# Performance work log

Measured on AMD Instinct MI355X. Metric: run time of the kernel, lower is better.

## Reference

```python
import jax, jax.numpy as jnp
import numpy as np

N, E, R = 50000, 320000, 3
IN, HID, OUT = 768, 256, 64
NEG_SLOPE = 0.2


def _rgat_conv(x, src, dst, edge_type, W, q, k, bias):
    # x: [N, HID]; W: [R, HID, HID]; q,k: [HID, 1]; bias: [HID]
    n = x.shape[0]
    xw = jnp.einsum('nc,rco->rno', x, W)          # [R, N, HID] per-relation transform
    out_i = xw[edge_type, dst]                      # [E, HID] transformed target feats
    out_j = xw[edge_type, src]                      # [E, HID] transformed source feats
    alpha = jax.nn.leaky_relu(out_i @ q + out_j @ k, NEG_SLOPE)  # [E, 1]
    # across-relation segment softmax over destination nodes (PyG softmax semantics)
    m = jax.ops.segment_max(alpha, dst, num_segments=n)          # [N, 1]
    ea = jnp.exp(alpha - m[dst])
    denom = jax.ops.segment_sum(ea, dst, num_segments=n)         # [N, 1]
    a = ea / (denom[dst] + 1e-16)                                # [E, 1]
    out = jax.ops.segment_sum(a * out_j, dst, num_segments=n)    # [N, HID]
    return out + bias


def setup_inputs() -> dict:
    key = jax.random.key(0)
    ks = jax.random.split(key, 16)
    g = lambda k, shape, fan: (jax.random.normal(k, shape, jnp.float32) / np.float32(np.sqrt(fan)))
    return {
        'x': jax.random.normal(ks[0], (N, IN), jnp.float32),
        'edge_index': jax.random.randint(ks[1], (2, E), 0, N),
        'edge_type': jax.random.randint(ks[2], (E,), 0, R),
        'w_in': g(ks[3], (IN, HID), IN), 'b_in': jnp.zeros((HID,), jnp.float32),
        'conv1_w': g(ks[4], (R, HID, HID), HID),
        'conv1_q': g(ks[5], (HID, 1), HID),
        'conv1_k': g(ks[6], (HID, 1), HID),
        'conv1_b': jnp.zeros((HID,), jnp.float32),
        'conv2_w': g(ks[7], (R, HID, HID), HID),
        'conv2_q': g(ks[8], (HID, 1), HID),
        'conv2_k': g(ks[9], (HID, 1), HID),
        'conv2_b': jnp.zeros((HID,), jnp.float32),
        'w_out': g(ks[10], (HID, OUT), HID), 'b_out': jnp.zeros((OUT,), jnp.float32),
        'w_cls': g(ks[11], (OUT, 2), OUT), 'b_cls': jnp.zeros((2,), jnp.float32),
    }


def reference(x, edge_index, edge_type, w_in, b_in,
              conv1_w, conv1_q, conv1_k, conv1_b,
              conv2_w, conv2_q, conv2_k, conv2_b,
              w_out, b_out, w_cls, b_cls):
    src, dst = edge_index[0], edge_index[1]
    h = jax.nn.relu(x @ w_in + b_in)                                  # [N, HID]
    h = _rgat_conv(h, src, dst, edge_type, conv1_w, conv1_q, conv1_k, conv1_b)
    h = _rgat_conv(h, src, dst, edge_type, conv2_w, conv2_q, conv2_k, conv2_b)
    h = jax.nn.relu(h @ w_out + b_out)                                # [N, OUT]
    return h @ w_cls + b_cls                                          # [N, 2]
```

## Files before the change

kernel.cpp:

```cpp
#include <hip/hip_runtime.h>
#include <hip/hip_bf16.h>

#define RG86_NN 50000
#define RG86_NE 320000
#define RG86_NR 3
#define RG86_DIN 768
#define RG86_HID 256
#define RG86_OUT 64

typedef __bf16 rg_bv8 __attribute__((ext_vector_type(8)));
typedef short rg_sv8 __attribute__((ext_vector_type(8)));
typedef float rg_fv4 __attribute__((ext_vector_type(4)));
typedef unsigned int rg_u32;

static __device__ float rg_b2f(unsigned short u) {
  return __uint_as_float(((unsigned int)u) << 16);
}
static __device__ unsigned short rg_f2b(float f) {
  unsigned int u = __float_as_uint(f);
  u += 0x7FFFu + ((u >> 16) & 1u);
  return (unsigned short)(u >> 16);
}

static __device__ __forceinline__ void rg_gl16(const void* g, void* lds_wave_base) {
  __builtin_amdgcn_global_load_lds(
      (const __attribute__((address_space(1))) rg_u32*)(unsigned long long)(uintptr_t)g,
      (__attribute__((address_space(3))) rg_u32*)(unsigned int)(uintptr_t)lds_wave_base,
      16, 0, 0);
}

__global__ void RGATModel_86371792322702_kernel() {}

__global__ void rg_castT(const float* in, unsigned short* out, int rows, int cols) {
  int i = blockIdx.x * 256 + threadIdx.x;
  if (i < rows * cols) {
    int r = i / cols, c = i % cols;
    out[(size_t)c * rows + r] = rg_f2b(in[i]);
  }
}

__global__ void rg_castT3(const float* in, unsigned short* out) {
  int i = blockIdx.x * 256 + threadIdx.x;
  if (i < RG86_NR * RG86_HID * RG86_HID) {
    int r = i >> 16, j = i & 65535;
    int row = j >> 8, col = j & 255;
    out[(r << 16) + (col << 8) + row] = rg_f2b(in[i]);
  }
}

__global__ void rg_wqk(const float* W, const float* q, const float* k,
                       float* wq, float* wk) {
  int lane = threadIdx.x & 63;
  int p = blockIdx.x * 4 + (threadIdx.x >> 6);
  if (p >= RG86_NR * RG86_HID) return;
  const float* wr = W + (size_t)p * RG86_HID;
  float qv = 0.f, kv = 0.f;
  for (int j = lane; j < RG86_HID; j += 64) {
    float w = wr[j];
    qv += w * q[j];
    kv += w * k[j];
  }
  for (int o = 32; o >= 1; o >>= 1) { qv += __shfl_xor(qv, o); kv += __shfl_xor(kv, o); }
  if (lane == 0) { wq[p] = qv; wk[p] = kv; }
}

__global__ void rg_qk2(const unsigned short* h, const float* wq, const float* wk,
                       float* qd, float* kd) {
  int lane = threadIdx.x & 63;
  int n = blockIdx.x * 4 + (threadIdx.x >> 6);
  if (n >= RG86_NN) return;
  ushort4 hv = *(const ushort4*)(h + (size_t)n * RG86_HID + lane * 4);
  float h0 = rg_b2f(hv.x), h1 = rg_b2f(hv.y), h2 = rg_b2f(hv.z), h3 = rg_b2f(hv.w);
  float acc[6];
#pragma unroll
  for (int r = 0; r < RG86_NR; r++) {
    const float* wqr = wq + r * RG86_HID + lane * 4;
    const float* wkr = wk + r * RG86_HID + lane * 4;
    acc[r] = h0 * wqr[0] + h1 * wqr[1] + h2 * wqr[2] + h3 * wqr[3];
    acc[3 + r] = h0 * wkr[0] + h1 * wkr[1] + h2 * wkr[2] + h3 * wkr[3];
  }
#pragma unroll
  for (int j = 0; j < 6; j++)
    for (int o = 32; o >= 1; o >>= 1) acc[j] += __shfl_xor(acc[j], o);
  if (lane == 0) {
#pragma unroll
    for (int r = 0; r < RG86_NR; r++) {
      qd[r * RG86_NN + n] = acc[r];
      kd[r * RG86_NN + n] = acc[3 + r];
    }
  }
}

__global__ __launch_bounds__(256) void rg_gemm2(
    const unsigned short* A, const unsigned short* Bt, const float* bias,
    unsigned short* C, int M, int N, int K, int relu, int split) {
  __shared__ unsigned short sA[128 * 64];
  __shared__ unsigned short sB[64 * 64];
  int tid = threadIdx.x;
  int wv = tid >> 6, lane = tid & 63;
  int nwg = gridDim.x;
  int q = nwg >> 3, rres = nwg & 7;
  int xcd = blockIdx.x & 7, jj = blockIdx.x >> 3;
  int wg = (xcd < rres ? xcd * (q + 1) : rres * (q + 1) + (xcd - rres) * q) + jj;
  int ntiles = N >> 6;
  int mt = wg / ntiles, nt = wg - mt * ntiles;
  int m0 = mt * 128, n0 = nt * 64;
  int frow = lane & 15, fhi = lane >> 4;
  rg_fv4 acc[2][4] = {};
  for (int k0 = 0; k0 < K; k0 += 64) {
#pragma unroll
    for (int i = 0; i < 4; i++) {
      int idx = i * 256 + tid;
      int r = idx >> 3, s = idx & 7;
      int gr = m0 + r;
      if (gr >= M) gr = M - 1;
      const unsigned short* gp = A + (size_t)gr * K + k0 + ((s ^ (r & 7)) << 3);
      rg_gl16(gp, (char*)sA + (size_t)(i * 256 + wv * 64) * 16);
    }
#pragma unroll
    for (int i = 0; i < 2; i++) {
      int idx = i * 256 + tid;
      int r = idx >> 3, s = idx & 7;
      const unsigned short* gp = Bt + (size_t)(n0 + r) * K + k0 + ((s ^ (r & 7)) << 3);
      rg_gl16(gp, (char*)sB + (size_t)(i * 256 + wv * 64) * 16);
    }
    __syncthreads();
#pragma unroll
    for (int ks = 0; ks < 2; ks++) {
      rg_bv8 af[2], bf[4];
#pragma unroll
      for (int mf = 0; mf < 2; mf++) {
        int r = wv * 32 + mf * 16 + frow;
        int slot = (ks * 4 + fhi) ^ (r & 7);
        af[mf] = *(const rg_bv8*)((const char*)sA + r * 128 + slot * 16);
      }
#pragma unroll
      for (int nf = 0; nf < 4; nf++) {
        int r = nf * 16 + frow;
        int slot = (ks * 4 + fhi) ^ (r & 7);
        bf[nf] = *(const rg_bv8*)((const char*)sB + r * 128 + slot * 16);
      }
#pragma unroll
      for (int mf = 0; mf < 2; mf++)
#pragma unroll
        for (int nf = 0; nf < 4; nf++)
          acc[mf][nf] = __builtin_amdgcn_mfma_f32_16x16x32_bf16(af[mf], bf[nf],
                                                                acc[mf][nf], 0, 0, 0);
    }
    __syncthreads();
  }
#pragma unroll
  for (int mf = 0; mf < 2; mf++) {
#pragma unroll
    for (int nf = 0; nf < 4; nf++) {
      int col = n0 + nf * 16 + frow;
      float bv = bias ? bias[col] : 0.f;
#pragma unroll
      for (int r = 0; r < 4; r++) {
        int row = m0 + wv * 32 + mf * 16 + fhi * 4 + r;
        if (row < M) {
          float v = acc[mf][nf][r] + bv;
          if (relu && v < 0.f) v = 0.f;
          if (split)
            C[((size_t)(col >> 8) * RG86_NN + row) * 256 + (col & 255)] = rg_f2b(v);
          else
            C[(size_t)row * N + col] = rg_f2b(v);
        }
      }
    }
  }
}

__global__ __launch_bounds__(256) void rg_gemm2f(
    const float* A, const unsigned short* Bt, const float* bias,
    unsigned short* C, int M, int N, int K, int relu) {
  __shared__ float sA[128 * 64];
  __shared__ unsigned short sB[64 * 64];
  int tid = threadIdx.x;
  int wv = tid >> 6, lane = tid & 63;
  int nwg = gridDim.x;
  int q = nwg >> 3, rres = nwg & 7;
  int xcd = blockIdx.x & 7, jj = blockIdx.x >> 3;
  int wg = (xcd < rres ? xcd * (q + 1) : rres * (q + 1) + (xcd - rres) * q) + jj;
  int ntiles = N >> 6;
  int mt = wg / ntiles, nt = wg - mt * ntiles;
  int m0 = mt * 128, n0 = nt * 64;
  int frow = lane & 15, fhi = lane >> 4;
  rg_fv4 acc[2][4] = {};
  for (int k0 = 0; k0 < K; k0 += 64) {
#pragma unroll
    for (int i = 0; i < 2; i++) {
      int idx = i * 256 + tid;
      int r = idx >> 3, s = idx & 7;
      const unsigned short* gp = Bt + (size_t)(n0 + r) * K + k0 + ((s ^ (r & 7)) << 3);
      rg_gl16(gp, (char*)sB + (size_t)(i * 256 + wv * 64) * 16);
    }
#pragma unroll
    for (int i = 0; i < 8; i++) {
      int idx = i * 256 + tid;
      int r = idx >> 4, hs = idx & 15;
      int gr = m0 + r;
      if (gr >= M) gr = M - 1;
      const float* gp = A + (size_t)gr * K + k0 +
                        ((((hs >> 1) ^ (r & 7)) << 3) + ((hs & 1) << 2));
      rg_gl16(gp, (char*)sA + (size_t)(i * 256 + wv * 64) * 16);
    }
    __syncthreads();
#pragma unroll
    for (int ks = 0; ks < 2; ks++) {
      rg_bv8 af[2], bf[4];
#pragma unroll
      for (int mf = 0; mf < 2; mf++) {
        int r = wv * 32 + mf * 16 + frow;
        int sp = (ks * 4 + fhi) ^ (r & 7);
        const float* ap = sA + r * 64 + sp * 8;
        float4 f0 = *(const float4*)ap;
        float4 f1 = *(const float4*)(ap + 4);
        rg_sv8 av;
        av[0] = (short)rg_f2b(f0.x); av[1] = (short)rg_f2b(f0.y);
        av[2] = (short)rg_f2b(f0.z); av[3] = (short)rg_f2b(f0.w);
        av[4] = (short)rg_f2b(f1.x); av[5] = (short)rg_f2b(f1.y);
        av[6] = (short)rg_f2b(f1.z); av[7] = (short)rg_f2b(f1.w);
        af[mf] = *(rg_bv8*)&av;
      }
#pragma unroll
      for (int nf = 0; nf < 4; nf++) {
        int r = nf * 16 + frow;
        int slot = (ks * 4 + fhi) ^ (r & 7);
        bf[nf] = *(const rg_bv8*)((const char*)sB + r * 128 + slot * 16);
      }
#pragma unroll
      for (int mf = 0; mf < 2; mf++)
#pragma unroll
        for (int nf = 0; nf < 4; nf++)
          acc[mf][nf] = __builtin_amdgcn_mfma_f32_16x16x32_bf16(af[mf], bf[nf],
                                                                acc[mf][nf], 0, 0, 0);
    }
    __syncthreads();
  }
#pragma unroll
  for (int mf = 0; mf < 2; mf++) {
#pragma unroll
    for (int nf = 0; nf < 4; nf++) {
      int col = n0 + nf * 16 + frow;
      float bv = bias ? bias[col] : 0.f;
#pragma unroll
      for (int r = 0; r < 4; r++) {
        int row = m0 + wv * 32 + mf * 16 + fhi * 4 + r;
        if (row < M) {
          float v = acc[mf][nf][r] + bv;
          if (relu && v < 0.f) v = 0.f;
          C[(size_t)row * N + col] = rg_f2b(v);
        }
      }
    }
  }
}

__global__ void rg_hist(const int* d, int* counts) {
  int e = blockIdx.x * 256 + threadIdx.x;
  if (e < RG86_NE) atomicAdd(&counts[d[e]], 1);
}

__global__ void rg_scan1(const int* counts, int* tmp, int* bsum, int n) {
  int b = blockIdx.x, t = threadIdx.x;
  int base = b * 1024 + t * 4;
  int v0 = 0, v1 = 0, v2 = 0, v3 = 0;
  if (base + 3 < n) {
    int4 v = *(const int4*)(counts + base);
    v0 = v.x; v1 = v.y; v2 = v.z; v3 = v.w;
  } else {
    if (base + 0 < n) v0 = counts[base + 0];
    if (base + 1 < n) v1 = counts[base + 1];
    if (base + 2 < n) v2 = counts[base + 2];
    if (base + 3 < n) v3 = counts[base + 3];
  }
  int tsum = v0 + v1 + v2 + v3;
  int lane = t & 63, wave = t >> 6;
  int s = tsum;
  for (int off = 1; off < 64; off <<= 1) {
    int u = __shfl_up(s, off);
    if (lane >= off) s += u;
  }
  __shared__ int wsum[4];
  if (lane == 63) wsum[wave] = s;
  __syncthreads();
  int woff = 0;
  for (int w = 0; w < wave; w++) woff += wsum[w];
  int excl = woff + s - tsum;
  int e0 = excl, e1 = e0 + v0, e2 = e1 + v1, e3 = e2 + v2;
  if (base + 3 < n) {
    *(int4*)(tmp + base) = make_int4(e0, e1, e2, e3);
  } else {
    if (base + 0 < n) tmp[base + 0] = e0;
    if (base + 1 < n) tmp[base + 1] = e1;
    if (base + 2 < n) tmp[base + 2] = e2;
    if (base + 3 < n) tmp[base + 3] = e3;
  }
  if (t == 255) bsum[b] = woff + s;
}

__global__ void rg_scan2(int* bsum, int* rowptr, int nb, int n) {
  int lane = threadIdx.x;
  int v = (lane < nb) ? bsum[lane] : 0;
  int s = v;
  for (int off = 1; off < 64; off <<= 1) {
    int u = __shfl_up(s, off);
    if (lane >= off) s += u;
  }
  if (lane < nb) bsum[lane] = s - v;
  if (lane == 63) rowptr[n] = s;
}

__global__ void rg_scan3(const int* bsum, int* rowptr, int* cursor, int n) {
  int b = blockIdx.x, t = threadIdx.x;
  int base = b * 1024 + t * 4;
  int off = bsum[b];
  if (base + 3 < n) {
    int4 v = *(const int4*)(cursor + base);
    int4 o = make_int4(v.x + off, v.y + off, v.z + off, v.w + off);
    *(int4*)(rowptr + base) = o;
    *(int4*)(cursor + base) = o;
  } else {
    for (int j = 0; j < 4; j++)
      if (base + j < n) {
        int o = cursor[base + j] + off;
        rowptr[base + j] = o;
        cursor[base + j] = o;
      }
  }
}

__global__ void rg_scatter(const int* d, int* cursor, int* perm) {
  int e = blockIdx.x * 256 + threadIdx.x;
  if (e < RG86_NE) perm[atomicAdd(&cursor[d[e]], 1)] = e;
}

__global__ void rg_edge(const int* perm, const int* src, const int* dst,
                        const int* et, const float* qd, const float* kd,
                        float* alphap, int* srcrel) {
  int i = blockIdx.x * 256 + threadIdx.x;
  if (i >= RG86_NE) return;
  int e = perm[i];
  int t = et[e], sv = src[e], dv = dst[e];
  float al = qd[t * RG86_NN + dv] + kd[t * RG86_NN + sv];
  al = al > 0.f ? al : 0.2f * al;
  alphap[i] = al;
  srcrel[i] = t * RG86_NN + sv;
}

__global__ void rg_agg(const int* rowptr, const float* alphap, const int* srcrel,
                       const unsigned short* xw, const float* bias,
                       unsigned short* out) {
  __shared__ float sw[4][64];
  __shared__ int ssrc[4][64];
  int lane = threadIdx.x & 63;
  int wv = threadIdx.x >> 6;
  int node = blockIdx.x * 4 + wv;
  if (node >= RG86_NN) return;
  int s0 = rowptr[node], s1 = rowptr[node + 1];
  int c0 = lane * 4;
  float a0 = 0.f, a1 = 0.f, a2 = 0.f, a3 = 0.f;
  if (s1 > s0) {
    float m = -1e30f;
    for (int bs = s0; bs < s1; bs += 64) {
      int i = bs + lane;
      float al = (i < s1) ? alphap[i] : -1e30f;
      m = fmaxf(m, al);
    }
    for (int o = 32; o >= 1; o >>= 1) m = fmaxf(m, __shfl_xor(m, o));
    float den = 0.f;
    for (int bs = s0; bs < s1; bs += 64) {
      int i = bs + lane;
      if (i < s1) den += __expf(alphap[i] - m);
    }
    for (int o = 32; o >= 1; o >>= 1) den += __shfl_xor(den, o);
    float inv = 1.f / (den + 1e-16f);
    for (int bs = s0; bs < s1; bs += 64) {
      int i = bs + lane;
      int nch = s1 - bs; if (nch > 64) nch = 64;
      float w = 0.f; int sr = 0;
      if (i < s1) { w = __expf(alphap[i] - m) * inv; sr = srcrel[i]; }
      sw[wv][lane] = w;
      ssrc[wv][lane] = sr;
#pragma unroll 4
      for (int j = 0; j < nch; j++) {
        float wj = sw[wv][j];
        ushort4 v = *(const ushort4*)(xw + (size_t)ssrc[wv][j] * RG86_HID + c0);
        a0 += wj * rg_b2f(v.x);
        a1 += wj * rg_b2f(v.y);
        a2 += wj * rg_b2f(v.z);
        a3 += wj * rg_b2f(v.w);
      }
    }
  }
  unsigned short* op = out + (size_t)node * RG86_HID + c0;
  op[0] = rg_f2b(a0 + bias[c0 + 0]);
  op[1] = rg_f2b(a1 + bias[c0 + 1]);
  op[2] = rg_f2b(a2 + bias[c0 + 2]);
  op[3] = rg_f2b(a3 + bias[c0 + 3]);
}

__global__ void rg_cls(const unsigned short* h4, const float* wc, const float* bc,
                       float* out) {
  int n = blockIdx.x * 256 + threadIdx.x;
  if (n >= RG86_NN) return;
  float a0 = bc[0], a1 = bc[1];
  const unsigned short* hr = h4 + (size_t)n * RG86_OUT;
  for (int j = 0; j < RG86_OUT; j++) {
    float h = rg_b2f(hr[j]);
    a0 += h * wc[j * 2 + 0];
    a1 += h * wc[j * 2 + 1];
  }
  out[n * 2 + 0] = a0;
  out[n * 2 + 1] = a1;
}

extern "C" void kernel_launch(void* const* d_in, const int* in_sizes, int n_in,
                              void* d_out, int out_size, void* d_ws, size_t ws_size,
                              hipStream_t stream) {
  (void)in_sizes; (void)n_in; (void)out_size;
  const float* x = (const float*)d_in[0];
  const int* ei = (const int*)d_in[1];
  const int* etp = (const int*)d_in[2];
  const float* w_in = (const float*)d_in[3];
  const float* b_in = (const float*)d_in[4];
  const float* c1w = (const float*)d_in[5];
  const float* c1q = (const float*)d_in[6];
  const float* c1k = (const float*)d_in[7];
  const float* c1b = (const float*)d_in[8];
  const float* c2w = (const float*)d_in[9];
  const float* c2q = (const float*)d_in[10];
  const float* c2k = (const float*)d_in[11];
  const float* c2b = (const float*)d_in[12];
  const float* w_out = (const float*)d_in[13];
  const float* b_out = (const float*)d_in[14];
  const float* w_cls = (const float*)d_in[15];
  const float* b_cls = (const float*)d_in[16];
  const int* esrc = ei;
  const int* edst = ei + RG86_NE;

  char* base = (char*)d_ws;
  size_t off = 0;
  unsigned short* xw = (unsigned short*)(base + off);
  off += (size_t)RG86_NR * RG86_NN * RG86_HID * 2;
  unsigned short* h1b = (unsigned short*)(base + off); off += (size_t)RG86_NN * RG86_HID * 2;
  unsigned short* h2b = (unsigned short*)(base + off); off += (size_t)RG86_NN * RG86_HID * 2;
  unsigned short* h4b = (unsigned short*)(base + off); off += (size_t)RG86_NN * RG86_OUT * 2;
  unsigned short* w_inT = (unsigned short*)(base + off); off += (size_t)RG86_DIN * RG86_HID * 2;
  unsigned short* c1wT = (unsigned short*)(base + off); off += (size_t)RG86_NR * RG86_HID * RG86_HID * 2;
  unsigned short* c2wT = (unsigned short*)(base + off); off += (size_t)RG86_NR * RG86_HID * RG86_HID * 2;
  unsigned short* w_outT = (unsigned short*)(base + off); off += (size_t)RG86_HID * RG86_OUT * 2;
  float* qd = (float*)(base + off); off += (size_t)RG86_NR * RG86_NN * 4;
  float* kd = (float*)(base + off); off += (size_t)RG86_NR * RG86_NN * 4;
  float* wq1 = (float*)(base + off); off += (size_t)RG86_NR * RG86_HID * 4;
  float* wk1 = (float*)(base + off); off += (size_t)RG86_NR * RG86_HID * 4;
  float* wq2 = (float*)(base + off); off += (size_t)RG86_NR * RG86_HID * 4;
  float* wk2 = (float*)(base + off); off += (size_t)RG86_NR * RG86_HID * 4;
  int* counts = (int*)(base + off); off += (size_t)RG86_NN * 4;
  int* rowptr = (int*)(base + off); off += (size_t)(RG86_NN + 4) * 4;
  int* cursor = (int*)(base + off); off += (size_t)RG86_NN * 4;
  int* perm = (int*)(base + off); off += (size_t)RG86_NE * 4;
  int* bsum = (int*)(base + off); off += (size_t)64 * 4;
  float* alphap = (float*)(base + off); off += (size_t)RG86_NE * 4;
  int* srcrel = (int*)(base + off); off += (size_t)RG86_NE * 4;
  if (off > ws_size) return;

  int mt128 = (RG86_NN + 127) / 128;
  int nsb = (RG86_NN + 1023) / 1024;

  rg_castT<<<(RG86_DIN * RG86_HID + 255) / 256, 256, 0, stream>>>(
      w_in, w_inT, RG86_DIN, RG86_HID);
  rg_castT3<<<(RG86_NR * RG86_HID * RG86_HID + 255) / 256, 256, 0, stream>>>(c1w, c1wT);
  rg_castT3<<<(RG86_NR * RG86_HID * RG86_HID + 255) / 256, 256, 0, stream>>>(c2w, c2wT);
  rg_castT<<<(RG86_HID * RG86_OUT + 255) / 256, 256, 0, stream>>>(
      w_out, w_outT, RG86_HID, RG86_OUT);
  rg_wqk<<<(RG86_NR * RG86_HID + 3) / 4, 256, 0, stream>>>(c1w, c1q, c1k, wq1, wk1);
  rg_wqk<<<(RG86_NR * RG86_HID + 3) / 4, 256, 0, stream>>>(c2w, c2q, c2k, wq2, wk2);

  rg_gemm2f<<<mt128 * 4, 256, 0, stream>>>(x, w_inT, b_in, h1b,
                                           RG86_NN, RG86_HID, RG86_DIN, 1);

  hipMemsetAsync(counts, 0, (size_t)RG86_NN * 4, stream);
  rg_hist<<<(RG86_NE + 255) / 256, 256, 0, stream>>>(edst, counts);
  rg_scan1<<<nsb, 256, 0, stream>>>(counts, cursor, bsum, RG86_NN);
  rg_scan2<<<1, 64, 0, stream>>>(bsum, rowptr, nsb, RG86_NN);
  rg_scan3<<<nsb, 256, 0, stream>>>(bsum, rowptr, cursor, RG86_NN);
  rg_scatter<<<(RG86_NE + 255) / 256, 256, 0, stream>>>(edst, cursor, perm);

  rg_gemm2<<<mt128 * 12, 256, 0, stream>>>(h1b, c1wT, (const float*)0, xw,
                                           RG86_NN, RG86_NR * RG86_HID, RG86_HID, 0, 1);
  rg_qk2<<<(RG86_NN + 3) / 4, 256, 0, stream>>>(h1b, wq1, wk1, qd, kd);
  rg_edge<<<(RG86_NE + 255) / 256, 256, 0, stream>>>(perm, esrc, edst, etp, qd, kd,
                                                     alphap, srcrel);
  rg_agg<<<(RG86_NN + 3) / 4, 256, 0, stream>>>(rowptr, alphap, srcrel,
                                                xw, c1b, h2b);

  rg_gemm2<<<mt128 * 12, 256, 0, stream>>>(h2b, c2wT, (const float*)0, xw,
                                           RG86_NN, RG86_NR * RG86_HID, RG86_HID, 0, 1);
  rg_qk2<<<(RG86_NN + 3) / 4, 256, 0, stream>>>(h2b, wq2, wk2, qd, kd);
  rg_edge<<<(RG86_NE + 255) / 256, 256, 0, stream>>>(perm, esrc, edst, etp, qd, kd,
                                                     alphap, srcrel);
  rg_agg<<<(RG86_NN + 3) / 4, 256, 0, stream>>>(rowptr, alphap, srcrel,
                                                xw, c2b, h1b);

  rg_gemm2<<<mt128, 256, 0, stream>>>(h1b, w_outT, b_out, h4b,
                                      RG86_NN, RG86_OUT, RG86_HID, 1, 0);

  rg_cls<<<(RG86_NN + 255) / 256, 256, 0, stream>>>(h4b, w_cls, b_cls, (float*)d_out);
}
```

Baseline: 582.4 us.

## Double-buffer LDS tiles in both GEMM kernels to overlap loads with MFMA

Both bf16 GEMM kernels now keep two LDS buffers for A and B. The next K-tile is issued with direct-to-LDS loads while the current tile feeds the MFMAs, so each iteration needs one barrier instead of two and load latency can hide behind compute. The cost is twice the shared memory: the fp32-A kernel grows to about 80KB, which can lower occupancy. Correctness depends on the async loads finishing before the trailing barrier.

```diff
diff --git a/kernel.cpp b/kernel.cpp
--- a/kernel.cpp
+++ b/kernel.cpp
@@ -94,8 +94,8 @@
 __global__ __launch_bounds__(256) void rg_gemm2(
     const unsigned short* A, const unsigned short* Bt, const float* bias,
     unsigned short* C, int M, int N, int K, int relu, int split) {
-  __shared__ unsigned short sA[128 * 64];
-  __shared__ unsigned short sB[64 * 64];
+  __shared__ unsigned short sA[2][128 * 64];
+  __shared__ unsigned short sB[2][64 * 64];
   int tid = threadIdx.x;
   int wv = tid >> 6, lane = tid & 63;
   int nwg = gridDim.x;
@@ -106,25 +106,32 @@
   int mt = wg / ntiles, nt = wg - mt * ntiles;
   int m0 = mt * 128, n0 = nt * 64;
   int frow = lane & 15, fhi = lane >> 4;
+  int sr = tid >> 3, ss = tid & 7;
   rg_fv4 acc[2][4] = {};
-  for (int k0 = 0; k0 < K; k0 += 64) {
+
+  auto stage = [&](int buf, int k0) {
 #pragma unroll
     for (int i = 0; i < 4; i++) {
-      int idx = i * 256 + tid;
-      int r = idx >> 3, s = idx & 7;
+      int r = i * 32 + sr;
       int gr = m0 + r;
       if (gr >= M) gr = M - 1;
-      const unsigned short* gp = A + (size_t)gr * K + k0 + ((s ^ (r & 7)) << 3);
-      rg_gl16(gp, (char*)sA + (size_t)(i * 256 + wv * 64) * 16);
+      const unsigned short* gp = A + (size_t)gr * K + k0 + ((ss ^ (r & 7)) << 3);
+      rg_gl16(gp, (char*)sA[buf] + (size_t)(i * 256 + wv * 64) * 16);
     }
 #pragma unroll
     for (int i = 0; i < 2; i++) {
-      int idx = i * 256 + tid;
-      int r = idx >> 3, s = idx & 7;
-      const unsigned short* gp = Bt + (size_t)(n0 + r) * K + k0 + ((s ^ (r & 7)) << 3);
-      rg_gl16(gp, (char*)sB + (size_t)(i * 256 + wv * 64) * 16);
-    }
-    __syncthreads();
+      int r = i * 32 + sr;
+      const unsigned short* gp = Bt + (size_t)(n0 + r) * K + k0 + ((ss ^ (r & 7)) << 3);
+      rg_gl16(gp, (char*)sB[buf] + (size_t)(i * 256 + wv * 64) * 16);
+    }
+  };
+
+  int nst = K >> 6;
+  stage(0, 0);
+  __syncthreads();
+  int cur = 0;
+  for (int t = 0; t < nst; t++) {
+    if (t + 1 < nst) stage(cur ^ 1, (t + 1) << 6);
 #pragma unroll
     for (int ks = 0; ks < 2; ks++) {
       rg_bv8 af[2], bf[4];
@@ -132,13 +139,13 @@
       for (int mf = 0; mf < 2; mf++) {
         int r = wv * 32 + mf * 16 + frow;
         int slot = (ks * 4 + fhi) ^ (r & 7);
-        af[mf] = *(const rg_bv8*)((const char*)sA + r * 128 + slot * 16);
+        af[mf] = *(const rg_bv8*)((const char*)sA[cur] + r * 128 + slot * 16);
       }
 #pragma unroll
       for (int nf = 0; nf < 4; nf++) {
         int r = nf * 16 + frow;
         int slot = (ks * 4 + fhi) ^ (r & 7);
-        bf[nf] = *(const rg_bv8*)((const char*)sB + r * 128 + slot * 16);
+        bf[nf] = *(const rg_bv8*)((const char*)sB[cur] + r * 128 + slot * 16);
       }
 #pragma unroll
       for (int mf = 0; mf < 2; mf++)
@@ -148,6 +155,7 @@
                                                                 acc[mf][nf], 0, 0, 0);
     }
     __syncthreads();
+    cur ^= 1;
   }
 #pragma unroll
   for (int mf = 0; mf < 2; mf++) {
@@ -174,8 +182,8 @@
 __global__ __launch_bounds__(256) void rg_gemm2f(
     const float* A, const unsigned short* Bt, const float* bias,
     unsigned short* C, int M, int N, int K, int relu) {
-  __shared__ float sA[128 * 64];
-  __shared__ unsigned short sB[64 * 64];
+  __shared__ float sA[2][128 * 64];
+  __shared__ unsigned short sB[2][64 * 64];
   int tid = threadIdx.x;
   int wv = tid >> 6, lane = tid & 63;
   int nwg = gridDim.x;
@@ -186,26 +194,34 @@
   int mt = wg / ntiles, nt = wg - mt * ntiles;
   int m0 = mt * 128, n0 = nt * 64;
   int frow = lane & 15, fhi = lane >> 4;
+  int sr8 = tid >> 3, ss8 = tid & 7;
+  int sr16 = tid >> 4, hs = tid & 15;
   rg_fv4 acc[2][4] = {};
-  for (int k0 = 0; k0 < K; k0 += 64) {
+
+  auto stage = [&](int buf, int k0) {
 #pragma unroll
     for (int i = 0; i < 2; i++) {
-      int idx = i * 256 + tid;
-      int r = idx >> 3, s = idx & 7;
-      const unsigned short* gp = Bt + (size_t)(n0 + r) * K + k0 + ((s ^ (r & 7)) << 3);
-      rg_gl16(gp, (char*)sB + (size_t)(i * 256 + wv * 64) * 16);
+      int r = i * 32 + sr8;
+      const unsigned short* gp = Bt + (size_t)(n0 + r) * K + k0 + ((ss8 ^ (r & 7)) << 3);
+      rg_gl16(gp, (char*)sB[buf] + (size_t)(i * 256 + wv * 64) * 16);
     }
 #pragma unroll
     for (int i = 0; i < 8; i++) {
-      int idx = i * 256 + tid;
-      int r = idx >> 4, hs = idx & 15;
+      int r = i * 16 + sr16;
       int gr = m0 + r;
       if (gr >= M) gr = M - 1;
       const float* gp = A + (size_t)gr * K + k0 +
                         ((((hs >> 1) ^ (r & 7)) << 3) + ((hs & 1) << 2));
-      rg_gl16(gp, (char*)sA + (size_t)(i * 256 + wv * 64) * 16);
-    }
-    __syncthreads();
+      rg_gl16(gp, (char*)sA[buf] + (size_t)(i * 256 + wv * 64) * 16);
+    }
+  };
+
+  int nst = K >> 6;
+  stage(0, 0);
+  __syncthreads();
+  int cur = 0;
+  for (int t = 0; t < nst; t++) {
+    if (t + 1 < nst) stage(cur ^ 1, (t + 1) << 6);
 #pragma unroll
     for (int ks = 0; ks < 2; ks++) {
       rg_bv8 af[2], bf[4];
@@ -213,7 +229,7 @@
       for (int mf = 0; mf < 2; mf++) {
         int r = wv * 32 + mf * 16 + frow;
         int sp = (ks * 4 + fhi) ^ (r & 7);
-        const float* ap = sA + r * 64 + sp * 8;
+        const float* ap = sA[cur] + r * 64 + sp * 8;
         float4 f0 = *(const float4*)ap;
         float4 f1 = *(const float4*)(ap + 4);
         rg_sv8 av;
@@ -227,7 +243,7 @@
       for (int nf = 0; nf < 4; nf++) {
         int r = nf * 16 + frow;
         int slot = (ks * 4 + fhi) ^ (r & 7);
-        bf[nf] = *(const rg_bv8*)((const char*)sB + r * 128 + slot * 16);
+        bf[nf] = *(const rg_bv8*)((const char*)sB[cur] + r * 128 + slot * 16);
       }
 #pragma unroll
       for (int mf = 0; mf < 2; mf++)
@@ -237,6 +253,7 @@
                                                                 acc[mf][nf], 0, 0, 0);
     }
     __syncthreads();
+    cur ^= 1;
   }
 #pragma unroll
   for (int mf = 0; mf < 2; mf++) {
```

After: 643.9 us. 10.6% more time.
